# Performance work log

Measured on AMD Instinct MI355X. Metric: run time of the kernel, lower is better.

The kernel has to match this reference:

```python
import jax, jax.numpy as jnp
import numpy as np

H = W = 64
C = 256
NUM_HEADS = 8

# Static index maps from AbsolutePositionalWeighting.__init__
_center_h = (H - 1) // 2
_center_w = (W - 1) // 2
_gi, _gj = np.meshgrid(np.arange(H), np.arange(W), indexing='ij')
_dx = _gi - _center_h
_dy = _gj - _center_w
DH = max(int(np.abs(_dx).max()), _center_h)
DW = max(int(np.abs(_dy).max()), _center_w)
DX_IDX = jnp.asarray(_dx + DH)  # (H, W)
DY_IDX = jnp.asarray(_dy + DW)  # (H, W)


def setup_inputs() -> dict:
    key = jax.random.key(0)
    ks = jax.random.split(key, 6)
    B, N = 16, H * W
    x1 = jax.random.normal(ks[0], (B, N, C), dtype=jnp.float32)
    x2 = jax.random.normal(ks[1], (B, N, C), dtype=jnp.float32)
    x3 = jax.random.normal(ks[2], (B, N, C), dtype=jnp.float32)
    pos_weights = 0.1 * jax.random.normal(ks[3], (2 * DH + 1, 2 * DW + 1, C), dtype=jnp.float32)
    lepe_w = 0.1 * jax.random.normal(ks[4], (C, 1, 3, 3), dtype=jnp.float32)  # depthwise OIHW
    lepe_b = 0.01 * jax.random.normal(ks[5], (C,), dtype=jnp.float32)
    return {"x1": x1, "x2": x2, "x3": x3, "pos_weights": pos_weights,
            "lepe_w": lepe_w, "lepe_b": lepe_b}


def reference(x1, x2, x3, pos_weights, lepe_w, lepe_b):
    b, n, c = x1.shape
    nh, hd = NUM_HEADS, c // NUM_HEADS

    q = jax.nn.elu(x1) + 1.0
    k = jax.nn.elu(x2) + 1.0
    v = x3

    # Positional gating: sigmoid(pos_weights gathered at per-pixel offsets) -> (N, C)
    pw = jax.nn.sigmoid(pos_weights[DX_IDX, DY_IDX, :]).reshape(n, c)
    q_rope = q * pw[None]  # (b, n, c)
    k_rope = k * pw[None]

    # Split heads: (b, n, nh, hd)
    q4 = q.reshape(b, n, nh, hd)
    k4 = k.reshape(b, n, nh, hd)
    v4 = v.reshape(b, n, nh, hd)
    qr4 = q_rope.reshape(b, n, nh, hd)
    kr4 = k_rope.reshape(b, n, nh, hd)

    # Normalizer z = 1 / (q . mean_n(k) + eps)
    k_mean = k4.mean(axis=1)  # (b, nh, hd)
    z = 1.0 / (jnp.einsum('bnhd,bhd->bnh', q4, k_mean) + 1e-6)

    # Linear attention: kv = (k_rope/sqrt(n))^T (v/sqrt(n)); out = q_rope @ kv * z
    kv = jnp.einsum('bnhd,bnhe->bhde', kr4, v4) / n  # (b, nh, hd, hd)
    attn = jnp.einsum('bnhd,bhde->bnhe', qr4, kv) * z[..., None]
    attn = attn.reshape(b, n, c)

    # LePE: depthwise 3x3 conv on v image (NCHW)
    v_img = v.reshape(b, H, W, c).transpose(0, 3, 1, 2)
    lepe = jax.lax.conv_general_dilated(
        v_img, lepe_w, window_strides=(1, 1), padding='SAME',
        feature_group_count=c,
        dimension_numbers=('NCHW', 'OIHW', 'NCHW'))
    lepe = lepe + lepe_b[None, :, None, None]
    lepe = lepe.transpose(0, 2, 3, 1).reshape(b, n, c)

    return attn + lepe
```

## Files before the change

### kernel.cpp

```cpp
#include <hip/hip_runtime.h>

#define BB 16
#define HIMG 64
#define WIMG 64
#define CC 256
#define NHEAD 8
#define HD 32
#define NN 4096
#define PWD 65

__device__ __forceinline__ float elu1(float x) {
    return x > 0.0f ? x + 1.0f : __expf(x);
}
__device__ __forceinline__ float sigm(float x) {
    return 1.0f / (1.0f + __expf(-x));
}

__global__ __launch_bounds__(256) void k0_pw(
    const float* __restrict__ posw, float* __restrict__ pw)
{
    const int gid = blockIdx.x * 256 + threadIdx.x;
    const int n = gid >> 6;
    const int p = gid & 63;
    const int ii = n >> 6, jj = n & 63;
    const float4 v = *(const float4*)(posw + (size_t)((ii + 1) * PWD + (jj + 1)) * CC + p * 4);
    float4 r;
    r.x = sigm(v.x); r.y = sigm(v.y); r.z = sigm(v.z); r.w = sigm(v.w);
    *(float4*)(pw + (size_t)n * CC + p * 4) = r;
}

__global__ __launch_bounds__(256) void k1_partial(
    const float* __restrict__ x2, const float* __restrict__ x3,
    const float* __restrict__ pw, float* __restrict__ pkv,
    float* __restrict__ pksum, int nchl, int rows)
{
    const int blk   = blockIdx.x;
    const int b     = blk >> nchl;
    const int chunk = blk & ((1 << nchl) - 1);
    const int n0    = chunk * rows;
    const int t     = threadIdx.x;
    const int p     = t & 127;
    const int pp    = p - 64;
    const int rbase = t >> 7;

    const int h   = t >> 5;
    const int idx = t & 31;
    const int dt  = idx & 7;
    const int et  = idx >> 3;

    __shared__ float kr_lds[2][4][CC];
    __shared__ float v_lds[2][4][CC];
    __shared__ float ksum_lds[2][CC];

    float acc[4][8];
#pragma unroll
    for (int a = 0; a < 4; ++a)
#pragma unroll
        for (int e = 0; e < 8; ++e) acc[a][e] = 0.0f;
    float ks0 = 0.f, ks1 = 0.f, ks2 = 0.f, ks3 = 0.f;

    const float* x2b = x2 + (size_t)b * NN * CC;
    const float* x3b = x3 + (size_t)b * NN * CC;

    const int nstep = rows >> 2;
    float4 kx[2], pv[2], vx[2];

    {
        const int r0 = n0;
        if (p < 64) {
#pragma unroll
            for (int it = 0; it < 2; ++it) {
                const int n = r0 + rbase + 2 * it;
                kx[it] = *(const float4*)(x2b + (size_t)n * CC + p * 4);
            }
#pragma unroll
            for (int it = 0; it < 2; ++it) {
                const int n = r0 + rbase + 2 * it;
                pv[it] = *(const float4*)(pw + (size_t)n * CC + p * 4);
            }
        } else {
#pragma unroll
            for (int it = 0; it < 2; ++it) {
                const int n = r0 + rbase + 2 * it;
                vx[it] = *(const float4*)(x3b + (size_t)n * CC + pp * 4);
            }
        }
    }

    int buf = 0;
    for (int s = 0; s < nstep; ++s) {
        if (p < 64) {
#pragma unroll
            for (int it = 0; it < 2; ++it) {
                const int row = rbase + 2 * it;
                float4 kk;
                kk.x = elu1(kx[it].x); kk.y = elu1(kx[it].y);
                kk.z = elu1(kx[it].z); kk.w = elu1(kx[it].w);
                float4 kr;
                kr.x = kk.x * pv[it].x; kr.y = kk.y * pv[it].y;
                kr.z = kk.z * pv[it].z; kr.w = kk.w * pv[it].w;
                *(float4*)(&kr_lds[buf][row][p * 4]) = kr;
                ks0 += kk.x; ks1 += kk.y; ks2 += kk.z; ks3 += kk.w;
            }
        } else {
#pragma unroll
            for (int it = 0; it < 2; ++it)
                *(float4*)(&v_lds[buf][rbase + 2 * it][pp * 4]) = vx[it];
        }
        __syncthreads();
        if (s + 1 < nstep) {
            const int r0 = n0 + (s + 1) * 4;
            if (p < 64) {
#pragma unroll
                for (int it = 0; it < 2; ++it) {
                    const int n = r0 + rbase + 2 * it;
                    kx[it] = *(const float4*)(x2b + (size_t)n * CC + p * 4);
                }
#pragma unroll
                for (int it = 0; it < 2; ++it) {
                    const int n = r0 + rbase + 2 * it;
                    pv[it] = *(const float4*)(pw + (size_t)n * CC + p * 4);
                }
            } else {
#pragma unroll
                for (int it = 0; it < 2; ++it) {
                    const int n = r0 + rbase + 2 * it;
                    vx[it] = *(const float4*)(x3b + (size_t)n * CC + pp * 4);
                }
            }
        }
#pragma unroll
        for (int r = 0; r < 4; ++r) {
            const float4 k4 = *(const float4*)(&kr_lds[buf][r][h * HD + dt * 4]);
            const float4 va = *(const float4*)(&v_lds[buf][r][h * HD + et * 8]);
            const float4 vb = *(const float4*)(&v_lds[buf][r][h * HD + et * 8 + 4]);
            const float kd[4] = {k4.x, k4.y, k4.z, k4.w};
            const float ve[8] = {va.x, va.y, va.z, va.w, vb.x, vb.y, vb.z, vb.w};
#pragma unroll
            for (int a = 0; a < 4; ++a)
#pragma unroll
                for (int e = 0; e < 8; ++e)
                    acc[a][e] = fmaf(kd[a], ve[e], acc[a][e]);
        }
        buf ^= 1;
    }

    if (p < 64) {
        ksum_lds[rbase][p * 4 + 0] = ks0;
        ksum_lds[rbase][p * 4 + 1] = ks1;
        ksum_lds[rbase][p * 4 + 2] = ks2;
        ksum_lds[rbase][p * 4 + 3] = ks3;
    }
    __syncthreads();
    pksum[(size_t)blk * CC + t] = ksum_lds[0][t] + ksum_lds[1][t];

    float* dst = pkv + (size_t)blk * (NHEAD * HD * HD);
#pragma unroll
    for (int a = 0; a < 4; ++a)
#pragma unroll
        for (int e = 0; e < 8; ++e)
            dst[h * (HD * HD) + (dt * 4 + a) * HD + (et * 8 + e)] = acc[a][e];
}

__global__ __launch_bounds__(256) void k2_reduce(
    const float* __restrict__ pkv, const float* __restrict__ pksum,
    float* __restrict__ kvf, float* __restrict__ kmean, int nch)
{
    const int gid = blockIdx.x * 256 + threadIdx.x;
    const int b = gid >> 13;
    const int o = gid & 8191;
    float s = 0.f;
#pragma unroll 4
    for (int c = 0; c < nch; ++c)
        s += pkv[(size_t)(b * nch + c) * (NHEAD * HD * HD) + o];
    kvf[gid] = s * (1.0f / NN);
    if (o < CC) {
        float ss = 0.f;
#pragma unroll 4
        for (int c = 0; c < nch; ++c)
            ss += pksum[(size_t)(b * nch + c) * CC + o];
        kmean[b * CC + o] = ss * (1.0f / NN);
    }
}

__global__ __launch_bounds__(256, 3) void k3_out(
    const float* __restrict__ x1, const float* __restrict__ x3,
    const float* __restrict__ pw, const float* __restrict__ kvf,
    const float* __restrict__ kmean, const float* __restrict__ lw,
    const float* __restrict__ lb, float* __restrict__ out)
{
    const int blk  = blockIdx.x;
    const int b    = blk >> 8;
    const int irow = (blk >> 2) & 63;
    const int jq   = blk & 3;
    const int j0   = jq << 4;
    const int t    = threadIdx.x;
    const int h    = t >> 5;
    const int e    = t & 31;

    __shared__ float qr_lds[16][CC];
    __shared__ float z_lds[16][8];

    float kvc[HD];
    {
        const float* kp = kvf + (size_t)b * (NHEAD * HD * HD) + h * (HD * HD) + e;
#pragma unroll
        for (int d = 0; d < HD; ++d) kvc[d] = kp[d * HD];
    }
    float wreg[9];
#pragma unroll
    for (int q = 0; q < 9; ++q) wreg[q] = lw[t * 9 + q];
    const float bias = lb[t];

    {
        const int p    = t & 63;
        const int pixo = t >> 6;
        const int hh   = p >> 3;
        const float4 km4 = *(const float4*)(kmean + b * CC + p * 4);
        const float* x1b = x1 + ((size_t)b * NN + (size_t)irow * 64 + j0) * CC;
        const float* pwb = pw + ((size_t)irow * 64 + j0) * CC;
        float4 xv[4], pvv[4];
#pragma unroll
        for (int s = 0; s < 4; ++s)
            xv[s] = *(const float4*)(x1b + (size_t)(s * 4 + pixo) * CC + p * 4);
#pragma unroll
        for (int s = 0; s < 4; ++s)
            pvv[s] = *(const float4*)(pwb + (size_t)(s * 4 + pixo) * CC + p * 4);
#pragma unroll
        for (int s = 0; s < 4; ++s) {
            const int pix = s * 4 + pixo;
            float4 q4;
            q4.x = elu1(xv[s].x); q4.y = elu1(xv[s].y);
            q4.z = elu1(xv[s].z); q4.w = elu1(xv[s].w);
            float4 qr4;
            qr4.x = q4.x * pvv[s].x; qr4.y = q4.y * pvv[s].y;
            qr4.z = q4.z * pvv[s].z; qr4.w = q4.w * pvv[s].w;
            *(float4*)(&qr_lds[pix][p * 4]) = qr4;
            float zp = q4.x * km4.x + q4.y * km4.y + q4.z * km4.z + q4.w * km4.w;
            zp += __shfl_xor(zp, 1);
            zp += __shfl_xor(zp, 2);
            zp += __shfl_xor(zp, 4);
            if ((p & 7) == 0) z_lds[pix][hh] = 1.0f / (zp + 1e-6f);
        }
    }
    __syncthreads();

    const bool hasU = irow > 0, hasD = irow < 63;
    const float* rU = x3 + ((size_t)b * NN + (size_t)(irow - 1) * 64 + j0) * CC + t;
    const float* rM = x3 + ((size_t)b * NN + (size_t)irow * 64 + j0) * CC + t;
    const float* rD = x3 + ((size_t)b * NN + (size_t)(irow + 1) * 64 + j0) * CC + t;
    float* ob = out + ((size_t)b * NN + (size_t)irow * 64 + j0) * CC + t;

    float cu[2][10], cm[2][10], cd[2][10];
#pragma unroll
    for (int tt = 0; tt < 2; ++tt)
#pragma unroll
        for (int q = 0; q < 10; ++q) {
            const int col = tt * 8 + q - 1;
            const int g   = j0 + col;
            const bool ok = (g >= 0) && (g < 64);
            const long off = (long)col * CC;
            cm[tt][q] = ok ? rM[off] : 0.f;
            cu[tt][q] = (ok && hasU) ? rU[off] : 0.f;
            cd[tt][q] = (ok && hasD) ? rD[off] : 0.f;
        }

#pragma unroll
    for (int tt = 0; tt < 2; ++tt) {
#pragma unroll
        for (int q = 0; q < 8; ++q) {
            const int jl = tt * 8 + q;
            float lepe = bias
                + wreg[0] * cu[tt][q] + wreg[1] * cu[tt][q + 1] + wreg[2] * cu[tt][q + 2]
                + wreg[3] * cm[tt][q] + wreg[4] * cm[tt][q + 1] + wreg[5] * cm[tt][q + 2]
                + wreg[6] * cd[tt][q] + wreg[7] * cd[tt][q + 1] + wreg[8] * cd[tt][q + 2];

            const float* qrow = &qr_lds[jl][h * HD];
            float a0 = 0.f, a1 = 0.f;
#pragma unroll
            for (int d4 = 0; d4 < 4; ++d4) {
                const float4 qa = *(const float4*)(qrow + d4 * 4);
                const float4 qb = *(const float4*)(qrow + 16 + d4 * 4);
                a0 = fmaf(qa.x, kvc[d4 * 4 + 0], a0);
                a0 = fmaf(qa.y, kvc[d4 * 4 + 1], a0);
                a0 = fmaf(qa.z, kvc[d4 * 4 + 2], a0);
                a0 = fmaf(qa.w, kvc[d4 * 4 + 3], a0);
                a1 = fmaf(qb.x, kvc[16 + d4 * 4 + 0], a1);
                a1 = fmaf(qb.y, kvc[16 + d4 * 4 + 1], a1);
                a1 = fmaf(qb.z, kvc[16 + d4 * 4 + 2], a1);
                a1 = fmaf(qb.w, kvc[16 + d4 * 4 + 3], a1);
            }
            __builtin_nontemporal_store((a0 + a1) * z_lds[jl][h] + lepe,
                                        ob + (long)jl * CC);
        }
    }
}

extern "C" void kernel_launch(void* const* d_in, const int* in_sizes, int n_in,
                              void* d_out, int out_size, void* d_ws, size_t ws_size,
                              hipStream_t stream) {
    const float* x1   = (const float*)d_in[0];
    const float* x2   = (const float*)d_in[1];
    const float* x3   = (const float*)d_in[2];
    const float* posw = (const float*)d_in[3];
    const float* lw   = (const float*)d_in[4];
    const float* lb   = (const float*)d_in[5];
    float* out = (float*)d_out;

    const size_t pw_sz = (size_t)NN * CC;
    const size_t need64 = (pw_sz + (size_t)16 * 64 * 8192 + (size_t)16 * 64 * 256 +
                           (size_t)16 * 8192 + 16 * 256) * sizeof(float);
    const int nchl = (ws_size >= need64) ? 6 : 5;
    const int nch  = 1 << nchl;
    const int rows = NN >> nchl;

    float* pwb   = (float*)d_ws;
    float* pkv   = pwb + pw_sz;
    float* pksum = pkv + (size_t)16 * nch * 8192;
    float* kvf   = pksum + (size_t)16 * nch * 256;
    float* kmean = kvf + (size_t)16 * 8192;

    k0_pw<<<1024, 256, 0, stream>>>(posw, pwb);
    k1_partial<<<16 * nch, 256, 0, stream>>>(x2, x3, pwb, pkv, pksum, nchl, rows);
    k2_reduce<<<512, 256, 0, stream>>>(pkv, pksum, kvf, kmean, nch);
    k3_out<<<BB * 256, 256, 0, stream>>>(x1, x3, pwb, kvf, kmean, lw, lb, out);
}
```

Baseline: 102.1 us.

## Compute q_rope·kv with bf16 MFMA in output kernel, storing kv transposed bf16

The reduction kernel now writes the per-head kv matrix transposed and rounded to bf16. The output kernel folds the normalizer z into q_rope, stores it as bf16 in padded LDS, and runs a 16x16x32 bf16 MFMA per head-half instead of per-thread scalar FMA dot products. Results go through an fp32 LDS tile before being added to LePE and stored. This drops the 32-register kv column per thread and the scalar FMA loop, at the cost of bf16 rounding error, an extra barrier, and lower launch-bounds occupancy (2 instead of 3).

Result: no change. 100.7 us (-1.4%).

```diff
diff --git a/kernel.cpp b/kernel.cpp
--- a/kernel.cpp
+++ b/kernel.cpp
@@ -8,12 +8,21 @@
 #define HD 32
 #define NN 4096
 #define PWD 65
+#define PADC 264
+
+typedef short bf16x8 __attribute__((ext_vector_type(8)));
+typedef float f32x4 __attribute__((ext_vector_type(4)));
 
 __device__ __forceinline__ float elu1(float x) {
     return x > 0.0f ? x + 1.0f : __expf(x);
 }
 __device__ __forceinline__ float sigm(float x) {
     return 1.0f / (1.0f + __expf(-x));
+}
+__device__ __forceinline__ unsigned short f2bf(float f) {
+    union { float f; unsigned int u; } v; v.f = f;
+    unsigned int r = v.u + 0x7FFFu + ((v.u >> 16) & 1u);
+    return (unsigned short)(r >> 16);
 }
 
 __global__ __launch_bounds__(256) void k0_pw(
@@ -164,7 +173,7 @@
 
 __global__ __launch_bounds__(256) void k2_reduce(
     const float* __restrict__ pkv, const float* __restrict__ pksum,
-    float* __restrict__ kvf, float* __restrict__ kmean, int nch)
+    unsigned short* __restrict__ kvbT, float* __restrict__ kmean, int nch)
 {
     const int gid = blockIdx.x * 256 + threadIdx.x;
     const int b = gid >> 13;
@@ -173,7 +182,8 @@
 #pragma unroll 4
     for (int c = 0; c < nch; ++c)
         s += pkv[(size_t)(b * nch + c) * (NHEAD * HD * HD) + o];
-    kvf[gid] = s * (1.0f / NN);
+    const int hh = o >> 10, d = (o >> 5) & 31, e = o & 31;
+    kvbT[(((size_t)b * NHEAD + hh) * HD + e) * HD + d] = f2bf(s * (1.0f / NN));
     if (o < CC) {
         float ss = 0.f;
 #pragma unroll 4
@@ -183,9 +193,9 @@
     }
 }
 
-__global__ __launch_bounds__(256, 3) void k3_out(
+__global__ __launch_bounds__(256, 2) void k3_out(
     const float* __restrict__ x1, const float* __restrict__ x3,
-    const float* __restrict__ pw, const float* __restrict__ kvf,
+    const float* __restrict__ pw, const unsigned short* __restrict__ kvbT,
     const float* __restrict__ kmean, const float* __restrict__ lw,
     const float* __restrict__ lb, float* __restrict__ out)
 {
@@ -195,18 +205,10 @@
     const int jq   = blk & 3;
     const int j0   = jq << 4;
     const int t    = threadIdx.x;
-    const int h    = t >> 5;
-    const int e    = t & 31;
-
-    __shared__ float qr_lds[16][CC];
-    __shared__ float z_lds[16][8];
-
-    float kvc[HD];
-    {
-        const float* kp = kvf + (size_t)b * (NHEAD * HD * HD) + h * (HD * HD) + e;
-#pragma unroll
-        for (int d = 0; d < HD; ++d) kvc[d] = kp[d * HD];
-    }
+
+    __shared__ unsigned short qr_bf[16 * PADC];
+    __shared__ float attn_lds[16][CC];
+
     float wreg[9];
 #pragma unroll
     for (int q = 0; q < 9; ++q) wreg[q] = lw[t * 9 + q];
@@ -215,7 +217,6 @@
     {
         const int p    = t & 63;
         const int pixo = t >> 6;
-        const int hh   = p >> 3;
         const float4 km4 = *(const float4*)(kmean + b * CC + p * 4);
         const float* x1b = x1 + ((size_t)b * NN + (size_t)irow * 64 + j0) * CC;
         const float* pwb = pw + ((size_t)irow * 64 + j0) * CC;
@@ -232,24 +233,24 @@
             float4 q4;
             q4.x = elu1(xv[s].x); q4.y = elu1(xv[s].y);
             q4.z = elu1(xv[s].z); q4.w = elu1(xv[s].w);
-            float4 qr4;
-            qr4.x = q4.x * pvv[s].x; qr4.y = q4.y * pvv[s].y;
-            qr4.z = q4.z * pvv[s].z; qr4.w = q4.w * pvv[s].w;
-            *(float4*)(&qr_lds[pix][p * 4]) = qr4;
             float zp = q4.x * km4.x + q4.y * km4.y + q4.z * km4.z + q4.w * km4.w;
             zp += __shfl_xor(zp, 1);
             zp += __shfl_xor(zp, 2);
             zp += __shfl_xor(zp, 4);
-            if ((p & 7) == 0) z_lds[pix][hh] = 1.0f / (zp + 1e-6f);
-        }
-    }
-    __syncthreads();
+            const float zin = 1.0f / (zp + 1e-6f);
+            ushort4 u;
+            u.x = f2bf(q4.x * pvv[s].x * zin);
+            u.y = f2bf(q4.y * pvv[s].y * zin);
+            u.z = f2bf(q4.z * pvv[s].z * zin);
+            u.w = f2bf(q4.w * pvv[s].w * zin);
+            *(ushort4*)(&qr_bf[pix * PADC + p * 4]) = u;
+        }
+    }
 
     const bool hasU = irow > 0, hasD = irow < 63;
     const float* rU = x3 + ((size_t)b * NN + (size_t)(irow - 1) * 64 + j0) * CC + t;
     const float* rM = x3 + ((size_t)b * NN + (size_t)irow * 64 + j0) * CC + t;
     const float* rD = x3 + ((size_t)b * NN + (size_t)(irow + 1) * 64 + j0) * CC + t;
-    float* ob = out + ((size_t)b * NN + (size_t)irow * 64 + j0) * CC + t;
 
     float cu[2][10], cm[2][10], cd[2][10];
 #pragma unroll
@@ -265,6 +266,40 @@
             cd[tt][q] = (ok && hasD) ? rD[off] : 0.f;
         }
 
+    __syncthreads();
+
+    {
+        const int w  = t >> 6;
+        const int l  = t & 63;
+        const int lr = l & 15;
+        const int lg = l >> 4;
+
+        bf16x8 af0 = *(const bf16x8*)(&qr_bf[lr * PADC + (w * 2 + 0) * HD + lg * 8]);
+        bf16x8 af1 = *(const bf16x8*)(&qr_bf[lr * PADC + (w * 2 + 1) * HD + lg * 8]);
+
+        f32x4 acc[4];
+#pragma unroll
+        for (int ct = 0; ct < 4; ++ct) {
+            const int head = w * 2 + (ct >> 1);
+            const int cl   = (ct & 1) * 16 + lr;
+            const bf16x8 bf = *(const bf16x8*)(kvbT +
+                (((size_t)b * NHEAD + head) * HD + cl) * HD + lg * 8);
+            f32x4 z4 = {0.f, 0.f, 0.f, 0.f};
+            acc[ct] = __builtin_amdgcn_mfma_f32_16x16x32_bf16(
+                (ct < 2) ? af0 : af1, bf, z4, 0, 0, 0);
+        }
+#pragma unroll
+        for (int ct = 0; ct < 4; ++ct) {
+            const int c = (w * 2 + (ct >> 1)) * HD + (ct & 1) * 16 + lr;
+#pragma unroll
+            for (int r = 0; r < 4; ++r)
+                attn_lds[lg * 4 + r][c] = acc[ct][r];
+        }
+    }
+
+    __syncthreads();
+
+    float* ob = out + ((size_t)b * NN + (size_t)irow * 64 + j0) * CC + t;
 #pragma unroll
     for (int tt = 0; tt < 2; ++tt) {
 #pragma unroll
@@ -274,24 +309,7 @@
                 + wreg[0] * cu[tt][q] + wreg[1] * cu[tt][q + 1] + wreg[2] * cu[tt][q + 2]
                 + wreg[3] * cm[tt][q] + wreg[4] * cm[tt][q + 1] + wreg[5] * cm[tt][q + 2]
                 + wreg[6] * cd[tt][q] + wreg[7] * cd[tt][q + 1] + wreg[8] * cd[tt][q + 2];
-
-            const float* qrow = &qr_lds[jl][h * HD];
-            float a0 = 0.f, a1 = 0.f;
-#pragma unroll
-            for (int d4 = 0; d4 < 4; ++d4) {
-                const float4 qa = *(const float4*)(qrow + d4 * 4);
-                const float4 qb = *(const float4*)(qrow + 16 + d4 * 4);
-                a0 = fmaf(qa.x, kvc[d4 * 4 + 0], a0);
-                a0 = fmaf(qa.y, kvc[d4 * 4 + 1], a0);
-                a0 = fmaf(qa.z, kvc[d4 * 4 + 2], a0);
-                a0 = fmaf(qa.w, kvc[d4 * 4 + 3], a0);
-                a1 = fmaf(qb.x, kvc[16 + d4 * 4 + 0], a1);
-                a1 = fmaf(qb.y, kvc[16 + d4 * 4 + 1], a1);
-                a1 = fmaf(qb.z, kvc[16 + d4 * 4 + 2], a1);
-                a1 = fmaf(qb.w, kvc[16 + d4 * 4 + 3], a1);
-            }
-            __builtin_nontemporal_store((a0 + a1) * z_lds[jl][h] + lepe,
-                                        ob + (long)jl * CC);
+            __builtin_nontemporal_store(attn_lds[jl][t] + lepe, ob + (long)jl * CC);
         }
     }
 }
@@ -309,7 +327,8 @@
 
     const size_t pw_sz = (size_t)NN * CC;
     const size_t need64 = (pw_sz + (size_t)16 * 64 * 8192 + (size_t)16 * 64 * 256 +
-                           (size_t)16 * 8192 + 16 * 256) * sizeof(float);
+                           (size_t)16 * 256) * sizeof(float) +
+                          (size_t)16 * 8192 * sizeof(unsigned short);
     const int nchl = (ws_size >= need64) ? 6 : 5;
     const int nch  = 1 << nchl;
     const int rows = NN >> nchl;
@@ -317,11 +336,11 @@
     float* pwb   = (float*)d_ws;
     float* pkv   = pwb + pw_sz;
     float* pksum = pkv + (size_t)16 * nch * 8192;
-    float* kvf   = pksum + (size_t)16 * nch * 256;
-    float* kmean = kvf + (size_t)16 * 8192;
+    float* kmean = pksum + (size_t)16 * nch * 256;
+    unsigned short* kvbT = (unsigned short*)(kmean + (size_t)16 * 256);
 
     k0_pw<<<1024, 256, 0, stream>>>(posw, pwb);
     k1_partial<<<16 * nch, 256, 0, stream>>>(x2, x3, pwb, pkv, pksum, nchl, rows);
-    k2_reduce<<<512, 256, 0, stream>>>(pkv, pksum, kvf, kmean, nch);
-    k3_out<<<BB * 256, 256, 0, stream>>>(x1, x3, pwb, kvf, kmean, lw, lb, out);
-}
+    k2_reduce<<<512, 256, 0, stream>>>(pkv, pksum, kvbT, kmean, nch);
+    k3_out<<<BB * 256, 256, 0, stream>>>(x1, x3, pwb, kvbT, kmean, lw, lb, out);
+}
```
